# Kernel tuning notes

Measured on AMD Instinct MI355X. Metric: run time of the kernel, lower is better.

## Reference

```python
import jax, jax.numpy as jnp
import numpy as np
import math

B, S, HID = 2, 2048, 1152
NH, NKV = 16, 4
HD = HID // NH  # 72
GROUPS = NH // NKV  # 4
ROPE_BASE = 10000.0


def setup_inputs() -> dict:
    key = jax.random.key(0)
    ks = jax.random.split(key, 5)
    hidden_states = jax.random.normal(ks[0], (B, S, HID), dtype=jnp.float32)
    # causal additive mask: 0 on/below diagonal, -1e9 above
    causal = jnp.tril(jnp.ones((S, S), dtype=jnp.bool_))
    attention_mask = jnp.where(causal, 0.0, -1e9).astype(jnp.float32)[None, None]
    scale = 0.02
    wq = jax.random.normal(ks[1], (HID, HID), dtype=jnp.float32) * scale
    wk = jax.random.normal(ks[2], (NKV * HD, HID), dtype=jnp.float32) * scale
    wv = jax.random.normal(ks[3], (NKV * HD, HID), dtype=jnp.float32) * scale
    wo = jax.random.normal(ks[4], (HID, HID), dtype=jnp.float32) * scale
    return {"hidden_states": hidden_states, "attention_mask": attention_mask,
            "wq": wq, "wk": wk, "wv": wv, "wo": wo}


def _rotate_half(x):
    x1, x2 = jnp.split(x, 2, axis=-1)
    return jnp.concatenate((-x2, x1), axis=-1)


def _rope_cos_sin(seq_len, dim, dtype):
    inv_freq = 1.0 / (ROPE_BASE ** (jnp.arange(0, dim, 2, dtype=jnp.float32) / dim))
    t = jnp.arange(seq_len, dtype=jnp.float32)
    freqs = jnp.outer(t, inv_freq)          # [S, dim/2]
    emb = jnp.concatenate((freqs, freqs), axis=-1)  # [S, dim]
    return jnp.cos(emb).astype(dtype), jnp.sin(emb).astype(dtype)


def reference(hidden_states, attention_mask, wq, wk, wv, wo):
    b, s, _ = hidden_states.shape
    # projections (nn.Linear: x @ W.T)
    q = (hidden_states @ wq.T).reshape(b, s, NH, HD).transpose(0, 2, 1, 3)    # [b,nh,s,hd]
    k = (hidden_states @ wk.T).reshape(b, s, NKV, HD).transpose(0, 2, 1, 3)   # [b,nkv,s,hd]
    v = (hidden_states @ wv.T).reshape(b, s, NKV, HD).transpose(0, 2, 1, 3)
    # RoPE
    cos, sin = _rope_cos_sin(s, HD, hidden_states.dtype)
    cos, sin = cos[None, None], sin[None, None]  # [1,1,s,hd]
    q = q * cos + _rotate_half(q) * sin
    k = k * cos + _rotate_half(k) * sin
    # expand kv heads (repeat_interleave over head dim)
    k = jnp.repeat(k, GROUPS, axis=1)  # [b,nh,s,hd]
    v = jnp.repeat(v, GROUPS, axis=1)
    scores = jnp.einsum('bhqd,bhkd->bhqk', q, k) / math.sqrt(HD)
    scores = scores + attention_mask
    attn = jax.nn.softmax(scores.astype(jnp.float32), axis=-1).astype(q.dtype)
    out = jnp.einsum('bhqk,bhkd->bhqd', attn, v)
    out = out.transpose(0, 2, 1, 3).reshape(b, s, HID)
    return out @ wo.T
```

## Files before the change

kernel.cpp:

```cpp
#include <hip/hip_runtime.h>
#include <hip/hip_bf16.h>
#include <cstddef>

#define B_   2
#define S_   2048
#define HID_ 1152
#define NH_  16
#define NKV_ 4
#define HD_  72
#define MTOT (B_ * S_)
#define KVDIM (NKV_ * HD_)

typedef float f32x4 __attribute__((ext_vector_type(4)));
typedef short bf16x8 __attribute__((ext_vector_type(8)));
typedef short s4v __attribute__((ext_vector_type(4)));

__device__ __forceinline__ float bf2f(short x) {
  unsigned int u = ((unsigned int)(unsigned short)x) << 16;
  return __builtin_bit_cast(float, u);
}
__device__ __forceinline__ short f2bf(float f) {
  unsigned int u = __builtin_bit_cast(unsigned int, f);
  u += 0x7fff + ((u >> 16) & 1);
  return (short)(u >> 16);
}

__device__ __forceinline__ float fast_exp2(float x) {
#if __has_builtin(__builtin_amdgcn_exp2f)
  return __builtin_amdgcn_exp2f(x);
#else
  return exp2f(x);
#endif
}

__device__ __forceinline__ void async16(const short* g, short* lds) {
  __builtin_amdgcn_global_load_lds((const __attribute__((address_space(1))) void*)g,
                                   (__attribute__((address_space(3))) void*)lds,
                                   16, 0, 0);
}

__global__ void k_cvt_all(const float4* __restrict__ s0, const float4* __restrict__ s1,
                          const float4* __restrict__ s2, const float4* __restrict__ s3,
                          const float4* __restrict__ s4,
                          s4v* __restrict__ d0, s4v* __restrict__ d1, s4v* __restrict__ d2,
                          s4v* __restrict__ d3, s4v* __restrict__ d4,
                          float2* __restrict__ tab, short* __restrict__ Vt,
                          int n0, int n1, int n2, int n3, int n4t) {
  int ncvt = n0 + n1 + n2 + n3 + n4t;
  int ntab = S_ * 36;
  int total = ncvt + ntab + 32768;
  for (int i = blockIdx.x * blockDim.x + threadIdx.x; i < total;
       i += gridDim.x * blockDim.x) {
    if (i < ncvt) {
      const float4* s;
      s4v* d;
      int off = i;
      bool perm = false;
      if (off < n0) { s = s0; d = d0; }
      else {
        off -= n0;
        if (off < n1) { s = s1; d = d1; perm = true; }
        else {
          off -= n1;
          if (off < n2) { s = s2; d = d2; perm = true; }
          else {
            off -= n2;
            if (off < n3) { s = s3; d = d3; }
            else { off -= n3; s = s4; d = d4; }
          }
        }
      }
      float4 v = s[off];
      s4v o = { f2bf(v.x), f2bf(v.y), f2bf(v.z), f2bf(v.w) };
      int out = off;
      if (perm) {
        int r = off / 288, k4 = off - r * 288;
        int hh = r / 72, ii = r - hh * 72;
        int pr = hh * 72 + (ii < 36 ? 2 * ii : 2 * (ii - 36) + 1);
        out = pr * 288 + k4;
      }
      d[out] = o;
    } else if (i < ncvt + ntab) {
      int idx = i - ncvt;
      int ii = idx % 36, s = idx / 36;
      float freq = powf(10000.0f, -(float)ii / 36.0f);
      float a = (float)s * freq;
      tab[idx] = make_float2(cosf(a), sinf(a));
    } else {
      int idx2 = i - ncvt - ntab;
      int t = idx2 << 2;
      int sp = t & 2047;
      int rest = t >> 11;
      int dr = rest & 7;
      int bkv = rest >> 3;
      s4v val = {};
      if (dr == 0) { val[0] = (short)0x3F80; val[1] = (short)0x3F80;
                     val[2] = (short)0x3F80; val[3] = (short)0x3F80; }
      *(s4v*)(Vt + (size_t)bkv * 163840 + (size_t)(72 + dr) * 2048 + sp) = val;
    }
  }
}

#define BM 128
#define BN 128
#define BK 32

__global__ __launch_bounds__(256) void k_gemm_qkv(const short* __restrict__ A,
                                                  const short* __restrict__ Wq,
                                                  const short* __restrict__ Wk,
                                                  const short* __restrict__ Wv,
                                                  short* __restrict__ Qo,
                                                  short* __restrict__ Ko,
                                                  short* __restrict__ Vt,
                                                  const float2* __restrict__ tab) {
  const int K = HID_, NTOT = 1728;
  __shared__ short smem[16384];
  short* As0 = smem;
  short* Bs0 = smem + 4096;
  short* As1 = smem + 8192;
  short* Bs1 = smem + 12288;
  const int tid = threadIdx.x;
  const int l = tid & 63;
  const int w = tid >> 6;
  const int bm = blockIdx.x * BM;
  const int bn = blockIdx.y * BN;
  const int wr = (w >> 1) * 64;
  const int wc = (w & 1) * 64;
  const int c15 = l & 15, g = l >> 4;
  const int r0 = tid >> 2;
  const int c0 = (tid & 3) * 8;

  const short* srcA[2];
  const short* srcB[2];
#pragma unroll
  for (int it = 0; it < 2; ++it) {
    int ar = bm + it * 64 + r0;
    int br = bn + it * 64 + r0;
    if (br > NTOT - 1) br = NTOT - 1;
    const short* bsrc;
    if (br < 1152)      bsrc = Wq + (size_t)br * K;
    else if (br < 1440) bsrc = Wk + (size_t)(br - 1152) * K;
    else                bsrc = Wv + (size_t)(br - 1440) * K;
    srcA[it] = A + (size_t)ar * K + c0;
    srcB[it] = bsrc + c0;
  }

  auto STAGE = [&](short* Ad, short* Bd) {
#pragma unroll
    for (int it = 0; it < 2; ++it) {
      async16(srcA[it], &Ad[(it * 64 + r0) * BK + c0]);
      async16(srcB[it], &Bd[(it * 64 + r0) * BK + c0]);
      srcA[it] += BK;
      srcB[it] += BK;
    }
  };

  f32x4 acc[4][4] = {};

  STAGE(As0, Bs0);
  short *Ac = As0, *Bc = Bs0, *An = As1, *Bn = Bs1;

  for (int k0 = 0; k0 < K; k0 += BK) {
    asm volatile("s_waitcnt vmcnt(0)" ::: "memory");
    __builtin_amdgcn_sched_barrier(0);
    __syncthreads();
    if (k0 + BK < K) STAGE(An, Bn);

    bf16x8 af[4], bfr[4];
#pragma unroll
    for (int t = 0; t < 4; ++t) {
      af[t]  = *(const bf16x8*)&Ac[(wr + t * 16 + c15) * BK + g * 8];
      bfr[t] = *(const bf16x8*)&Bc[(wc + t * 16 + c15) * BK + g * 8];
    }
#pragma unroll
    for (int mt = 0; mt < 4; ++mt)
#pragma unroll
      for (int nt = 0; nt < 4; ++nt)
        acc[mt][nt] = __builtin_amdgcn_mfma_f32_16x16x32_bf16(af[mt], bfr[nt], acc[mt][nt], 0, 0, 0);

    short* t1 = Ac; Ac = An; An = t1;
    short* t2 = Bc; Bc = Bn; Bn = t2;
  }

#pragma unroll
  for (int mt = 0; mt < 4; ++mt)
#pragma unroll
    for (int nt = 0; nt < 4; ++nt) {
      int col = bn + wc + nt * 16 + c15;
      if (col < 1152) {
#pragma unroll
        for (int j = 0; j < 4; ++j) {
          int row = bm + wr + mt * 16 + g * 4 + j;
          Qo[(size_t)row * HID_ + col] = f2bf(acc[mt][nt][j]);
        }
      } else if (col < 1440) {
        int ch = col - 1152;
        int ii = (ch % 72) >> 1;
#pragma unroll
        for (int j = 0; j < 4; ++j) {
          int row = bm + wr + mt * 16 + g * 4 + j;
          float v = acc[mt][nt][j];
          float p = __shfl_xor(v, 1);
          float2 cs = tab[(size_t)(row & (S_ - 1)) * 36 + ii];
          float r = (c15 & 1) ? (v * cs.x + p * cs.y)
                              : (v * cs.x - p * cs.y);
          Ko[(size_t)row * KVDIM + ch] = f2bf(r);
        }
      } else if (col < NTOT) {
        int cv = col - 1440;
        int d = cv % 72, kvh = cv / 72;
        int row0 = bm + wr + mt * 16 + g * 4;
        int bkv = (row0 >> 11) * 4 + kvh;
        s4v out;
#pragma unroll
        for (int j = 0; j < 4; ++j) out[j] = f2bf(acc[mt][nt][j]);
        *(s4v*)(Vt + (size_t)bkv * 163840 + (size_t)d * 2048 + (row0 & 2047)) = out;
      }
    }
}

__global__ __launch_bounds__(256) void k_gemm_o(const short* __restrict__ A,
                                                const short* __restrict__ Bm,
                                                float* __restrict__ C,
                                                int M, int N, int K) {
  __shared__ short smem[16384];
  short* As0 = smem;
  short* Bs0 = smem + 4096;
  short* As1 = smem + 8192;
  short* Bs1 = smem + 12288;
  const int tid = threadIdx.x;
  const int l = tid & 63;
  const int w = tid >> 6;
  const int bm = blockIdx.x * BM;
  const int bn = blockIdx.y * BN;
  const int wr = (w >> 1) * 64;
  const int wc = (w & 1) * 64;
  const int c15 = l & 15, g = l >> 4;
  const int r0 = tid >> 2;
  const int c0 = (tid & 3) * 8;

  const short* srcA[2];
  const short* srcB[2];
#pragma unroll
  for (int it = 0; it < 2; ++it) {
    int ar = bm + it * 64 + r0;
    int br = bn + it * 64 + r0;
    if (br > N - 1) br = N - 1;
    srcA[it] = A + (size_t)ar * K + c0;
    srcB[it] = Bm + (size_t)br * K + c0;
  }

  auto STAGE = [&](short* Ad, short* Bd) {
#pragma unroll
    for (int it = 0; it < 2; ++it) {
      async16(srcA[it], &Ad[(it * 64 + r0) * BK + c0]);
      async16(srcB[it], &Bd[(it * 64 + r0) * BK + c0]);
      srcA[it] += BK;
      srcB[it] += BK;
    }
  };

  f32x4 acc[4][4] = {};

  STAGE(As0, Bs0);
  short *Ac = As0, *Bc = Bs0, *An = As1, *Bn = Bs1;

  for (int k0 = 0; k0 < K; k0 += BK) {
    asm volatile("s_waitcnt vmcnt(0)" ::: "memory");
    __builtin_amdgcn_sched_barrier(0);
    __syncthreads();
    if (k0 + BK < K) STAGE(An, Bn);

    bf16x8 af[4], bfr[4];
#pragma unroll
    for (int t = 0; t < 4; ++t) {
      af[t]  = *(const bf16x8*)&Ac[(wr + t * 16 + c15) * BK + g * 8];
      bfr[t] = *(const bf16x8*)&Bc[(wc + t * 16 + c15) * BK + g * 8];
    }
#pragma unroll
    for (int mt = 0; mt < 4; ++mt)
#pragma unroll
      for (int nt = 0; nt < 4; ++nt)
        acc[mt][nt] = __builtin_amdgcn_mfma_f32_16x16x32_bf16(af[mt], bfr[nt], acc[mt][nt], 0, 0, 0);

    short* t1 = Ac; Ac = An; An = t1;
    short* t2 = Bc; Bc = Bn; Bn = t2;
  }

#pragma unroll
  for (int mt = 0; mt < 4; ++mt)
#pragma unroll
    for (int nt = 0; nt < 4; ++nt)
#pragma unroll
      for (int j = 0; j < 4; ++j) {
        int row = bm + wr + mt * 16 + g * 4 + j;
        int col = bn + wc + nt * 16 + c15;
        if (col < N) C[(size_t)row * N + col] = acc[mt][nt][j];
      }
}

#define QB 16
#define KT 128

__global__ __launch_bounds__(256, 2) void k_flash(const short* __restrict__ Q,
                                                  const short* __restrict__ Kg,
                                                  const short* __restrict__ Vt,
                                                  short* __restrict__ O,
                                                  const float2* __restrict__ tab) {
  const int bid = blockIdx.x;
  const int bkv = bid & 7;
  const int qt = 127 - (bid >> 3);
  const int b = bkv >> 2, kv = bkv & 3;
  const int tid = threadIdx.x;
  const int w = tid >> 6, l = tid & 63;
  const int h = kv * 4 + w;
  const int q0 = qt * QB;
  const int c15 = l & 15, g = l >> 4;

  __shared__ short lds[38912];
  short* Ks0 = lds;
  short* Vs0 = lds + 9216;
  short* Ks1 = lds + 19456;
  short* Vs1 = lds + 28672;

  const float SCL = 0.117851130f * 1.4426950408889634f;
  const float SHIFT = 8.0f;

  const short* Qbase = Q + (size_t)(b * S_) * HID_ + h * HD_;
  const short* Kbase = Kg + (size_t)(b * S_) * KVDIM + kv * HD_;
  const short* Vbase = Vt + (size_t)bkv * 80 * S_;

  const int lane_k = c15 * 72 + g * 8;
  int lane_v[4];
#pragma unroll
  for (int ks2 = 0; ks2 < 4; ++ks2)
    lane_v[ks2] = c15 * 128 + (((ks2 * 4 + g) ^ c15) << 3);
  const int pbase = w * 2176;
  const int pw_off = pbase + (g * 4) * 136 + c15;
  const int pr_off = pbase + c15 * 136 + g * 8;

  bf16x8 qf[3];
  const bf16x8 zfrag = {0, 0, 0, 0, 0, 0, 0, 0};
  {
    int row = q0 + c15;
    const short* qrow = Qbase + (size_t)row * HID_;
    const float2* trow = tab + (size_t)row * 36;
#pragma unroll
    for (int ks = 0; ks < 3; ++ks) {
      int d0 = ks * 32 + g * 8;
      if (d0 < HD_) {
        bf16x8 raw = *(const bf16x8*)(qrow + d0);
        bf16x8 o;
#pragma unroll
        for (int e = 0; e < 8; e += 2) {
          float2 cs = trow[(d0 + e) >> 1];
          float x1 = bf2f(raw[e]), x2 = bf2f(raw[e + 1]);
          o[e]     = f2bf((x1 * cs.x - x2 * cs.y) * SCL);
          o[e + 1] = f2bf((x2 * cs.x + x1 * cs.y) * SCL);
        }
        qf[ks] = o;
      } else {
        qf[ks] = zfrag;
      }
    }
  }

  f32x4 accO[5] = {};

  const int nkt = (16 * qt + 143) >> 7;
  const int nfull = (16 * qt + 1) >> 7;

  auto STAGE = [&](int kb, short* Kd, short* Vd) {
    const short* kp = Kbase + (size_t)kb * KVDIM;
    const short* vp = Vbase + kb;
#pragma unroll
    for (int i = 0; i < 10; ++i) {
      int c = tid + 256 * i;
      if (c < 1152) {
        int row = c / 9, cc = c - row * 9;
        async16(kp + (size_t)row * KVDIM + cc * 8, &Kd[c * 8]);
      } else if (c < 2432) {
        int c2 = c - 1152;
        int row = c2 >> 4, slot = c2 & 15;
        async16(vp + (size_t)row * S_ + ((slot ^ (row & 15)) << 3), &Vd[c2 * 8]);
      }
    }
  };

  STAGE(0, Ks0, Vs0);
  short *Ksc = Ks0, *Vsc = Vs0, *Ksn = Ks1, *Vsn = Vs1;

  for (int kt = 0; kt < nkt; ++kt) {
    asm volatile("s_waitcnt vmcnt(0)" ::: "memory");
    __builtin_amdgcn_sched_barrier(0);
    __syncthreads();
    if (kt + 1 < nkt) STAGE((kt + 1) * KT, Ksn, Vsn);

    const int kbase = kt * KT;

    f32x4 sc[8] = {};
    __builtin_amdgcn_s_setprio(1);
#pragma unroll
    for (int ct = 0; ct < 8; ++ct)
#pragma unroll
      for (int ks = 0; ks < 3; ++ks) {
        bf16x8 kf = *(const bf16x8*)&Ksc[lane_k + ct * 1152 + ks * 32];
        sc[ct] = __builtin_amdgcn_mfma_f32_16x16x32_bf16(qf[ks], kf, sc[ct], 0, 0, 0);
      }
    __builtin_amdgcn_s_setprio(0);

    const int qrow = q0 + g * 4;
    if (kt >= nfull) {
#pragma unroll
      for (int ct = 0; ct < 8; ++ct) {
        int col = kbase + ct * 16 + c15;
#pragma unroll
        for (int j = 0; j < 4; ++j)
          if (col > qrow + j) sc[ct][j] = -1e30f;
      }
    }
#pragma unroll
    for (int ct = 0; ct < 8; ++ct)
#pragma unroll
      for (int j = 0; j < 4; ++j)
        sc[ct][j] = fast_exp2(sc[ct][j] - SHIFT);

    __syncthreads();
#pragma unroll
    for (int ct = 0; ct < 8; ++ct)
#pragma unroll
      for (int j = 0; j < 4; ++j)
        Ksc[pw_off + j * 136 + ct * 16] = f2bf(sc[ct][j]);
    asm volatile("s_waitcnt lgkmcnt(0)" ::: "memory");
    __builtin_amdgcn_sched_barrier(0);
    bf16x8 pa[4];
#pragma unroll
    for (int ks2 = 0; ks2 < 4; ++ks2)
      pa[ks2] = *(const bf16x8*)&Ksc[pr_off + ks2 * 32];

    __builtin_amdgcn_s_setprio(1);
#pragma unroll
    for (int dt = 0; dt < 5; ++dt) {
#pragma unroll
      for (int ks2 = 0; ks2 < 4; ++ks2) {
        bf16x8 vb = *(const bf16x8*)&Vsc[lane_v[ks2] + dt * 2048];
        accO[dt] = __builtin_amdgcn_mfma_f32_16x16x32_bf16(pa[ks2], vb, accO[dt], 0, 0, 0);
      }
    }
    __builtin_amdgcn_s_setprio(0);

    short* t1 = Ksc; Ksc = Ksn; Ksn = t1;
    short* t2 = Vsc; Vsc = Vsn; Vsn = t2;
  }

  float lj[4];
#pragma unroll
  for (int j = 0; j < 4; ++j)
    lj[j] = 1.0f / __shfl(accO[4][j], (l & 48) | 8);
#pragma unroll
  for (int dt = 0; dt < 5; ++dt) {
    int d = dt * 16 + c15;
    if (d < HD_) {
#pragma unroll
      for (int j = 0; j < 4; ++j) {
        int row = q0 + g * 4 + j;
        O[(size_t)(b * S_ + row) * HID_ + h * HD_ + d] = f2bf(accO[dt][j] * lj[j]);
      }
    }
  }
}

extern "C" void kernel_launch(void* const* d_in, const int* in_sizes, int n_in,
                              void* d_out, int out_size, void* d_ws, size_t ws_size,
                              hipStream_t stream) {
  const float* hs = (const float*)d_in[0];
  const float* wq = (const float*)d_in[2];
  const float* wk = (const float*)d_in[3];
  const float* wv = (const float*)d_in[4];
  const float* wo = (const float*)d_in[5];

  char* ws = (char*)d_ws;
  short* Xb  = (short*)(ws + 0);
  short* Qb  = (short*)(ws + 9437184);
  short* Kb  = (short*)(ws + 18874368);
  short* Vt  = (short*)(ws + 23592960);
  short* Ob  = (short*)(ws + 26214400);
  short* wqb = (short*)(ws + 35651584);
  short* wkb = (short*)(ws + 38305792);
  short* wvb = (short*)(ws + 38969344);
  short* wob = (short*)(ws + 39632896);
  float2* tab = (float2*)(ws + 42287104);

  k_cvt_all<<<2048, 256, 0, stream>>>(
      (const float4*)hs, (const float4*)wq, (const float4*)wk, (const float4*)wv,
      (const float4*)wo,
      (s4v*)Xb, (s4v*)wqb, (s4v*)wkb, (s4v*)wvb, (s4v*)wob, tab, Vt,
      MTOT * HID_ / 4, HID_ * HID_ / 4, KVDIM * HID_ / 4, KVDIM * HID_ / 4,
      HID_ * HID_ / 4);

  k_gemm_qkv<<<dim3(32, 14), 256, 0, stream>>>(Xb, wqb, wkb, wvb, Qb, Kb, Vt, tab);

  k_flash<<<1024, 256, 0, stream>>>(Qb, Kb, Vt, Ob, tab);

  k_gemm_o<<<dim3(32, 9), 256, 0, stream>>>(Ob, wob, (float*)d_out, MTOT, HID_, HID_);
}
```

Before: 109.5 us.

## Share K/V tiles across two adjacent query tiles per 512-thread flash block

The flash-attention kernel now launches 512-thread blocks in which two groups of four waves handle two adjacent 16-row query tiles for the same KV head. Each staged K/V tile is therefore reused by both query tiles, halving global-to-LDS staging per query row, and the block count drops to 512. The P scratch area per wave shrinks, so P is written and read back in two halves through LDS. The extra cost is that the group with the shorter causal range sits idle on its last iteration while the other group still needs the barriers, plus the added LDS round-trips and waits.

```diff
diff --git a/kernel.cpp b/kernel.cpp
--- a/kernel.cpp
+++ b/kernel.cpp
@@ -302,18 +302,21 @@
 #define QB 16
 #define KT 128
 
-__global__ __launch_bounds__(256, 2) void k_flash(const short* __restrict__ Q,
+__global__ __launch_bounds__(512, 2) void k_flash(const short* __restrict__ Q,
                                                   const short* __restrict__ Kg,
                                                   const short* __restrict__ Vt,
                                                   short* __restrict__ O,
                                                   const float2* __restrict__ tab) {
   const int bid = blockIdx.x;
   const int bkv = bid & 7;
-  const int qt = 127 - (bid >> 3);
+  const int sidx = bid >> 3;
+  const int qtp = (bid < 256) ? sidx : 95 - sidx;
   const int b = bkv >> 2, kv = bkv & 3;
   const int tid = threadIdx.x;
   const int w = tid >> 6, l = tid & 63;
-  const int h = kv * 4 + w;
+  const int grp = w >> 2, hw = w & 3;
+  const int h = kv * 4 + hw;
+  const int qt = 127 - 2 * qtp - grp;
   const int q0 = qt * QB;
   const int c15 = l & 15, g = l >> 4;
 
@@ -335,9 +338,9 @@
 #pragma unroll
   for (int ks2 = 0; ks2 < 4; ++ks2)
     lane_v[ks2] = c15 * 128 + (((ks2 * 4 + g) ^ c15) << 3);
-  const int pbase = w * 2176;
-  const int pw_off = pbase + (g * 4) * 136 + c15;
-  const int pr_off = pbase + c15 * 136 + g * 8;
+  const int pbase = w * 1152;
+  const int pw_off = pbase + (g * 4) * 72 + c15;
+  const int pr_off = pbase + c15 * 72 + g * 8;
 
   bf16x8 qf[3];
   const bf16x8 zfrag = {0, 0, 0, 0, 0, 0, 0, 0};
@@ -367,19 +370,20 @@
 
   f32x4 accO[5] = {};
 
-  const int nkt = (16 * qt + 143) >> 7;
+  const int nkt   = (16 * qt + 143) >> 7;
+  const int nkt_m = (16 * (127 - 2 * qtp) + 143) >> 7;
   const int nfull = (16 * qt + 1) >> 7;
 
   auto STAGE = [&](int kb, short* Kd, short* Vd) {
     const short* kp = Kbase + (size_t)kb * KVDIM;
     const short* vp = Vbase + kb;
 #pragma unroll
-    for (int i = 0; i < 10; ++i) {
-      int c = tid + 256 * i;
+    for (int i = 0; i < 5; ++i) {
+      int c = tid + 512 * i;
       if (c < 1152) {
         int row = c / 9, cc = c - row * 9;
         async16(kp + (size_t)row * KVDIM + cc * 8, &Kd[c * 8]);
-      } else if (c < 2432) {
+      } else if (c < 2320) {
         int c2 = c - 1152;
         int row = c2 >> 4, slot = c2 & 15;
         async16(vp + (size_t)row * S_ + ((slot ^ (row & 15)) << 3), &Vd[c2 * 8]);
@@ -390,64 +394,78 @@
   STAGE(0, Ks0, Vs0);
   short *Ksc = Ks0, *Vsc = Vs0, *Ksn = Ks1, *Vsn = Vs1;
 
-  for (int kt = 0; kt < nkt; ++kt) {
+  for (int kt = 0; kt < nkt_m; ++kt) {
+    const bool act = kt < nkt;
     asm volatile("s_waitcnt vmcnt(0)" ::: "memory");
     __builtin_amdgcn_sched_barrier(0);
     __syncthreads();
-    if (kt + 1 < nkt) STAGE((kt + 1) * KT, Ksn, Vsn);
-
-    const int kbase = kt * KT;
+    if (kt + 1 < nkt_m) STAGE((kt + 1) * KT, Ksn, Vsn);
 
     f32x4 sc[8] = {};
-    __builtin_amdgcn_s_setprio(1);
-#pragma unroll
-    for (int ct = 0; ct < 8; ++ct)
-#pragma unroll
-      for (int ks = 0; ks < 3; ++ks) {
-        bf16x8 kf = *(const bf16x8*)&Ksc[lane_k + ct * 1152 + ks * 32];
-        sc[ct] = __builtin_amdgcn_mfma_f32_16x16x32_bf16(qf[ks], kf, sc[ct], 0, 0, 0);
-      }
-    __builtin_amdgcn_s_setprio(0);
-
-    const int qrow = q0 + g * 4;
-    if (kt >= nfull) {
-#pragma unroll
-      for (int ct = 0; ct < 8; ++ct) {
-        int col = kbase + ct * 16 + c15;
+    if (act) {
+      const int kbase = kt * KT;
+      __builtin_amdgcn_s_setprio(1);
+#pragma unroll
+      for (int ct = 0; ct < 8; ++ct)
+#pragma unroll
+        for (int ks = 0; ks < 3; ++ks) {
+          bf16x8 kf = *(const bf16x8*)&Ksc[lane_k + ct * 1152 + ks * 32];
+          sc[ct] = __builtin_amdgcn_mfma_f32_16x16x32_bf16(qf[ks], kf, sc[ct], 0, 0, 0);
+        }
+      __builtin_amdgcn_s_setprio(0);
+
+      const int qrow = q0 + g * 4;
+      if (kt >= nfull) {
+#pragma unroll
+        for (int ct = 0; ct < 8; ++ct) {
+          int col = kbase + ct * 16 + c15;
+#pragma unroll
+          for (int j = 0; j < 4; ++j)
+            if (col > qrow + j) sc[ct][j] = -1e30f;
+        }
+      }
+#pragma unroll
+      for (int ct = 0; ct < 8; ++ct)
 #pragma unroll
         for (int j = 0; j < 4; ++j)
-          if (col > qrow + j) sc[ct][j] = -1e30f;
-      }
-    }
-#pragma unroll
-    for (int ct = 0; ct < 8; ++ct)
-#pragma unroll
-      for (int j = 0; j < 4; ++j)
-        sc[ct][j] = fast_exp2(sc[ct][j] - SHIFT);
+          sc[ct][j] = fast_exp2(sc[ct][j] - SHIFT);
+    }
 
     __syncthreads();
-#pragma unroll
-    for (int ct = 0; ct < 8; ++ct)
-#pragma unroll
-      for (int j = 0; j < 4; ++j)
-        Ksc[pw_off + j * 136 + ct * 16] = f2bf(sc[ct][j]);
-    asm volatile("s_waitcnt lgkmcnt(0)" ::: "memory");
-    __builtin_amdgcn_sched_barrier(0);
-    bf16x8 pa[4];
-#pragma unroll
-    for (int ks2 = 0; ks2 < 4; ++ks2)
-      pa[ks2] = *(const bf16x8*)&Ksc[pr_off + ks2 * 32];
-
-    __builtin_amdgcn_s_setprio(1);
-#pragma unroll
-    for (int dt = 0; dt < 5; ++dt) {
-#pragma unroll
-      for (int ks2 = 0; ks2 < 4; ++ks2) {
-        bf16x8 vb = *(const bf16x8*)&Vsc[lane_v[ks2] + dt * 2048];
-        accO[dt] = __builtin_amdgcn_mfma_f32_16x16x32_bf16(pa[ks2], vb, accO[dt], 0, 0, 0);
-      }
-    }
-    __builtin_amdgcn_s_setprio(0);
+    if (act) {
+#pragma unroll
+      for (int ct = 0; ct < 4; ++ct)
+#pragma unroll
+        for (int j = 0; j < 4; ++j)
+          Ksc[pw_off + j * 72 + ct * 16] = f2bf(sc[ct][j]);
+      asm volatile("s_waitcnt lgkmcnt(0)" ::: "memory");
+      __builtin_amdgcn_sched_barrier(0);
+      bf16x8 pa[4];
+      pa[0] = *(const bf16x8*)&Ksc[pr_off];
+      pa[1] = *(const bf16x8*)&Ksc[pr_off + 32];
+      asm volatile("s_waitcnt lgkmcnt(0)" ::: "memory");
+      __builtin_amdgcn_sched_barrier(0);
+#pragma unroll
+      for (int ct = 0; ct < 4; ++ct)
+#pragma unroll
+        for (int j = 0; j < 4; ++j)
+          Ksc[pw_off + j * 72 + ct * 16] = f2bf(sc[4 + ct][j]);
+      asm volatile("s_waitcnt lgkmcnt(0)" ::: "memory");
+      __builtin_amdgcn_sched_barrier(0);
+      pa[2] = *(const bf16x8*)&Ksc[pr_off];
+      pa[3] = *(const bf16x8*)&Ksc[pr_off + 32];
+
+      __builtin_amdgcn_s_setprio(1);
+#pragma unroll
+      for (int dt = 0; dt < 5; ++dt) {
+#pragma unroll
+        for (int ks2 = 0; ks2 < 4; ++ks2) {
+          bf16x8 vb = *(const bf16x8*)&Vsc[lane_v[ks2] + dt * 2048];
+          accO[dt] = __builtin_amdgcn_mfma_f32_16x16x32_bf16(pa[ks2], vb, accO[dt], 0, 0, 0);
+        }
+      }
+      __builtin_amdgcn_s_setprio(0);
+    }
 
     short* t1 = Ksc; Ksc = Ksn; Ksn = t1;
     short* t2 = Vsc; Vsc = Vsn; Vsn = t2;
@@ -500,7 +518,7 @@
 
   k_gemm_qkv<<<dim3(32, 14), 256, 0, stream>>>(Xb, wqb, wkb, wvb, Qb, Kb, Vt, tab);
 
-  k_flash<<<1024, 256, 0, stream>>>(Qb, Kb, Vt, Ob, tab);
+  k_flash<<<512, 512, 0, stream>>>(Qb, Kb, Vt, Ob, tab);
 
   k_gemm_o<<<dim3(32, 9), 256, 0, stream>>>(Ob, wob, (float*)d_out, MTOT, HID_, HID_);
 }
```

Result: no change. 109.1 us (-0.3%).
